# Optimization experiments

Measured on AMD Instinct MI355X. Metric: run time of the kernel, lower is better.

Reference implementation:

```python
import jax, jax.numpy as jnp
import numpy as np

NUM_EMBEDDINGS = 8192
EMBED_DIM = 64
NUM_BATCH = 4
N_VOX = 32768
EPS = 1e-10


def setup_inputs() -> dict:
    key = jax.random.key(0)
    k1, k2, k3, k4 = jax.random.split(key, 4)
    z_feats = jax.random.normal(k1, (N_VOX, EMBED_DIM), dtype=jnp.float32)
    batch_ids = jax.random.randint(k2, (N_VOX, 1), 0, NUM_BATCH)
    xyz = jax.random.randint(k3, (N_VOX, 3), 0, 64)
    z_coords = jnp.concatenate([batch_ids, xyz], axis=1).astype(jnp.int32)
    codebook = jax.random.normal(k4, (NUM_EMBEDDINGS, EMBED_DIM), dtype=jnp.float32)
    return {"z_feats": z_feats, "z_coords": z_coords, "codebook": codebook}


def reference(z_feats, z_coords, codebook):
    # squared euclidean distances [N, K]; argmin identical to torch.cdist argmin
    d2 = (jnp.sum(z_feats * z_feats, axis=1, keepdims=True)
          - 2.0 * (z_feats @ codebook.T)
          + jnp.sum(codebook * codebook, axis=1)[None, :])
    encoding_indices = jnp.argmin(d2, axis=1)              # [N]
    quantized = codebook[encoding_indices]                 # [N, D] gather

    # losses (gradient mode, use_ema_update=False)
    commitment_loss = jnp.mean((z_feats - jax.lax.stop_gradient(quantized)) ** 2)
    vq_loss = jnp.mean((quantized - jax.lax.stop_gradient(z_feats)) ** 2)

    # straight-through estimator
    quantized_st = z_feats + jax.lax.stop_gradient(quantized - z_feats)

    # per-sample codebook stats (vectorized over the batch dimension)
    batch_ids = z_coords[:, 0]
    counts = jnp.zeros((NUM_BATCH, NUM_EMBEDDINGS), jnp.float32).at[batch_ids, encoding_indices].add(1.0)
    per_sample_n = jnp.sum(counts, axis=1, keepdims=True)  # tokens per sample
    probs = counts / per_sample_n
    sample_entropy = -jnp.sum(probs * jnp.log(probs + EPS), axis=1)  # [B]
    avg_entropy = jnp.mean(sample_entropy)
    avg_perplexity = jnp.mean(jnp.exp(sample_entropy))
    avg_unique_count = jnp.mean(jnp.sum(counts > 0, axis=1).astype(jnp.float32))
    utilization_ratio = avg_unique_count / NUM_EMBEDDINGS * 100.0

    encoding_indices_st = encoding_indices.astype(jnp.float32)[:, None]
    return (quantized_st, vq_loss, commitment_loss, encoding_indices_st,
            avg_perplexity, avg_entropy, avg_unique_count, utilization_ratio)
```

## Files before the change

kernel.cpp:

```cpp
#include <hip/hip_runtime.h>
#include <math.h>

#define NUM_EMB 8192
#define DIM     64
#define NBATCH  4
#define NVOX    32768
#define TPB     256
#define NSPLIT  4
#define QENT    (NUM_EMB / NSPLIT)
#define CHUNK   128
#define CERT_EPS 0.015f
#define RCH     512

#define OFF_Q     0
#define OFF_VQ    2097152
#define OFF_COMM  2097153
#define OFF_IDX   2097154
#define OFF_PERP  2129922
#define OFF_ENT   2129923
#define OFF_UNIQ  2129924
#define OFF_UTIL  2129925

typedef __bf16 bf16x8 __attribute__((ext_vector_type(8)));
typedef float  f32x4  __attribute__((ext_vector_type(4)));

#define GLDS16(SRC, DST) __builtin_amdgcn_global_load_lds(                    \
        (const __attribute__((address_space(1))) void*)(SRC),                 \
        (__attribute__((address_space(3))) void*)(DST), 16, 0, 0)

__device__ __forceinline__ unsigned short f2bf(float f) {
    unsigned u = __float_as_uint(f);
    unsigned r = u + 0x7FFFu + ((u >> 16) & 1u);
    return (unsigned short)(r >> 16);
}
__device__ __forceinline__ float bf2f(unsigned short h) {
    return __uint_as_float(((unsigned)h) << 16);
}
__device__ __forceinline__ unsigned fmap(float f) {
    unsigned u = __float_as_uint(f);
    return (u & 0x80000000u) ? ~u : (u | 0x80000000u);
}

__global__ void prep_kernel(const float* __restrict__ cb,
                            unsigned short* __restrict__ cbh,
                            unsigned short* __restrict__ cbm,
                            float* __restrict__ cnp4,
                            unsigned* __restrict__ counts,
                            unsigned* __restrict__ misc,
                            unsigned long long* __restrict__ merge,
                            float* __restrict__ out) {
    int row = blockIdx.x * 4 + (threadIdx.x >> 6);
    int l   = threadIdx.x & 63;
    float f = cb[row * DIM + l];
    unsigned short hh = f2bf(f); float r1 = f - bf2f(hh);
    cbh[row * DIM + l] = hh;
    cbm[row * DIM + l] = f2bf(r1);
    float s = f * f;
#pragma unroll
    for (int o = 32; o > 0; o >>= 1) s += __shfl_xor(s, o, 64);
    if (l < 4) cnp4[row * 4 + l] = -0.5f * s;

    int gid = blockIdx.x * TPB + threadIdx.x;
    if (gid < NBATCH * NUM_EMB) counts[gid] = 0;
    if (gid >= 32768 && gid < 65536) merge[gid - 32768] = ~0ull;
    if (gid < 16) misc[gid] = 0;
    if (blockIdx.x == 0) {
        if (threadIdx.x < 2) out[OFF_VQ + threadIdx.x] = 0.f;
        if (threadIdx.x < 4) out[OFF_PERP + threadIdx.x] = 0.f;
    }
}

__global__ __launch_bounds__(TPB) void argmin_kernel(
        const float* __restrict__ z,
        const unsigned short* __restrict__ cbh,
        const unsigned short* __restrict__ cbm,
        const float* __restrict__ cnp4,
        float4* __restrict__ res) {
    __shared__ __align__(16) char lds[2 * CHUNK * 128 + CHUNK * 16];

    const int t  = threadIdx.x;
    const int l  = t & 63, w = t >> 6;
    const int lc = l & 15, lg = l >> 4;
    const int vb = blockIdx.x >> 2, qh = blockIdx.x & 3;
    const int ebase = qh * QENT;

    union U { bf16x8 v; unsigned short s[8]; };
    U Ah[2][2], Am[2][2];
#pragma unroll
    for (int set = 0; set < 2; ++set) {
        const float* zp = z + (size_t)(vb * 128 + w * 32 + set * 16 + lc) * DIM + lg * 8;
#pragma unroll
        for (int ks = 0; ks < 2; ++ks)
#pragma unroll
            for (int j = 0; j < 8; ++j) {
                float f = zp[ks * 32 + j];
                unsigned short hh = f2bf(f);
                Ah[set][ks].s[j] = hh;
                Am[set][ks].s[j] = f2bf(f - bf2f(hh));
            }
    }

    float m1[2][4], m2[2][4]; int ix[2][4];
#pragma unroll
    for (int set = 0; set < 2; ++set)
#pragma unroll
        for (int r = 0; r < 4; ++r) {
            m1[set][r] = -INFINITY; m2[set][r] = -INFINITY; ix[set][r] = 0;
        }

    const int b0 = (lc * 128 + lg * 16) ^ ((lc & 7) << 4);
    const int b1 = b0 ^ 64;
    const int cb0 = 2 * CHUNK * 128 + lc * 16;

    for (int ch = 0; ch < QENT / CHUNK; ++ch) {
        const char* sh = (const char*)cbh + (size_t)(ebase + ch * CHUNK) * 128;
        const char* sm = (const char*)cbm + (size_t)(ebase + ch * CHUNK) * 128;
#pragma unroll
        for (int j = 0; j < 4; ++j) {
            int lin = (j * 256 + t) * 16;
            int src = lin ^ (((lin >> 7) & 7) << 4);
            int dstb = lin - l * 16;
            GLDS16(sh + src, lds + dstb);
            GLDS16(sm + src, lds + 16384 + dstb);
        }
        if (t < 128) {
            int lin = t * 16;
            GLDS16((const char*)cnp4 + (size_t)(ebase + ch * CHUNK) * 16 + lin,
                   lds + 32768 + (lin - l * 16));
        }
        __syncthreads();

        int e0 = ebase + ch * CHUNK + lc;
        for (int tile = 0; tile < CHUNK / 16; ++tile) {
            bf16x8 bh0 = *(const bf16x8*)(lds + b0 + tile * 2048);
            bf16x8 bh1 = *(const bf16x8*)(lds + b1 + tile * 2048);
            bf16x8 bm0 = *(const bf16x8*)(lds + 16384 + b0 + tile * 2048);
            bf16x8 bm1 = *(const bf16x8*)(lds + 16384 + b1 + tile * 2048);
            f32x4  c0  = *(const f32x4*)(lds + cb0 + tile * 256);
            int eidx = e0 + tile * 16;
#pragma unroll
            for (int set = 0; set < 2; ++set) {
                f32x4 a = c0;
                a = __builtin_amdgcn_mfma_f32_16x16x32_bf16(Ah[set][0].v, bh0, a, 0, 0, 0);
                a = __builtin_amdgcn_mfma_f32_16x16x32_bf16(Am[set][0].v, bh0, a, 0, 0, 0);
                a = __builtin_amdgcn_mfma_f32_16x16x32_bf16(Ah[set][0].v, bm0, a, 0, 0, 0);
                a = __builtin_amdgcn_mfma_f32_16x16x32_bf16(Ah[set][1].v, bh1, a, 0, 0, 0);
                a = __builtin_amdgcn_mfma_f32_16x16x32_bf16(Am[set][1].v, bh1, a, 0, 0, 0);
                a = __builtin_amdgcn_mfma_f32_16x16x32_bf16(Ah[set][1].v, bm1, a, 0, 0, 0);
#pragma unroll
                for (int r = 0; r < 4; ++r) {
                    float v = a[r];
                    m2[set][r] = __builtin_amdgcn_fmed3f(v, m1[set][r], m2[set][r]);
                    if (v > m1[set][r]) { m1[set][r] = v; ix[set][r] = eidx; }
                }
            }
        }
        __syncthreads();
    }

#pragma unroll
    for (int set = 0; set < 2; ++set)
#pragma unroll
        for (int r = 0; r < 4; ++r) {
            float v1 = m1[set][r], v2 = m2[set][r]; int i1 = ix[set][r];
#pragma unroll
            for (int st = 1; st < 16; st <<= 1) {
                float o1 = __shfl_xor(v1, st, 16);
                float o2 = __shfl_xor(v2, st, 16);
                int   oi = __shfl_xor(i1, st, 16);
                float mn = fminf(v1, o1);
                v2 = fmaxf(fmaxf(v2, o2), mn);
                if (o1 > v1 || (o1 == v1 && oi < i1)) { v1 = o1; i1 = oi; }
            }
            if (lc == 0) {
                int vox = vb * 128 + w * 32 + set * 16 + lg * 4 + r;
                res[(size_t)qh * NVOX + vox] =
                    make_float4(v1, v2, __int_as_float(i1), 0.f);
            }
        }
}

__global__ void combine_kernel(const float4* __restrict__ res, float* __restrict__ out) {
    int vox = blockIdx.x * blockDim.x + threadIdx.x;
    float v1 = -INFINITY, v2 = -INFINITY; int idx = 0;
#pragma unroll
    for (int h = 0; h < NSPLIT; ++h) {
        float4 t4 = res[(size_t)h * NVOX + vox];
        float a1 = t4.x, a2 = t4.y; int ai = __float_as_int(t4.z);
        float mn = fminf(v1, a1);
        v2 = fmaxf(fmaxf(v2, a2), mn);
        if (a1 > v1) { v1 = a1; idx = ai; }
    }
    unsigned flag = (v1 - v2 < CERT_EPS) ? 0x80000000u : 0u;
    ((unsigned*)out)[OFF_IDX + vox] = (unsigned)idx | flag;
}

__global__ void gather_kernel(const float* __restrict__ z, const int* __restrict__ zc,
        const float* __restrict__ cb, float* __restrict__ out,
        unsigned* __restrict__ counts, float* __restrict__ sqsum,
        unsigned* __restrict__ list, unsigned* __restrict__ lcount) {
    int vox = blockIdx.x * blockDim.x + threadIdx.x;
    unsigned pk = ((unsigned*)out)[OFF_IDX + vox];
    float s = 0.f;
    if (pk & 0x80000000u) {
        unsigned pos = atomicAdd(lcount, 1u);
        list[pos] = vox;
    } else {
        unsigned idx = pk;
        const float4* crow = (const float4*)(cb + (size_t)idx * DIM);
        const float4* zrow = (const float4*)(z + (size_t)vox * DIM);
        float4* qrow = (float4*)(out + OFF_Q + (size_t)vox * DIM);
#pragma unroll
        for (int i = 0; i < DIM / 4; ++i) {
            float4 c4 = crow[i];
            float4 z4 = zrow[i];
            float dx = z4.x - c4.x, dy = z4.y - c4.y;
            float dz = z4.z - c4.z, dw = z4.w - c4.w;
            s += dx * dx + dy * dy + dz * dz + dw * dw;
            qrow[i] = c4;
        }
        out[OFF_IDX + vox] = (float)idx;
        atomicAdd(&counts[zc[vox * 4] * NUM_EMB + idx], 1u);
    }
#pragma unroll
    for (int o = 32; o > 0; o >>= 1) s += __shfl_down(s, o, 64);
    __shared__ float red[TPB / 64];
    if ((threadIdx.x & 63) == 0) red[threadIdx.x >> 6] = s;
    __syncthreads();
    if (threadIdx.x == 0)
        atomicAdd(sqsum, red[0] + red[1] + red[2] + red[3]);
}

__global__ void gatherF_kernel(const float* __restrict__ z, const int* __restrict__ zc,
        const float* __restrict__ cb, const float4* __restrict__ res,
        float* __restrict__ out, unsigned* __restrict__ counts,
        float* __restrict__ sqsum, unsigned* __restrict__ list,
        unsigned* __restrict__ lcount) {
    int vox = blockIdx.x * blockDim.x + threadIdx.x;
    float v1 = -INFINITY, v2 = -INFINITY; int idx = 0;
#pragma unroll
    for (int h = 0; h < NSPLIT; ++h) {
        float4 t4 = res[(size_t)h * NVOX + vox];
        float a1 = t4.x, a2 = t4.y; int ai = __float_as_int(t4.z);
        float mn = fminf(v1, a1);
        v2 = fmaxf(fmaxf(v2, a2), mn);
        if (a1 > v1) { v1 = a1; idx = ai; }
    }
    float s = 0.f;
    if (v1 - v2 < CERT_EPS) {
        unsigned pos = atomicAdd(lcount, 1u);
        list[pos] = vox;
    } else {
        const float4* crow = (const float4*)(cb + (size_t)idx * DIM);
        const float4* zrow = (const float4*)(z + (size_t)vox * DIM);
        float4* qrow = (float4*)(out + OFF_Q + (size_t)vox * DIM);
#pragma unroll
        for (int i = 0; i < DIM / 4; ++i) {
            float4 c4 = crow[i];
            float4 z4 = zrow[i];
            float dx = z4.x - c4.x, dy = z4.y - c4.y;
            float dz = z4.z - c4.z, dw = z4.w - c4.w;
            s += dx * dx + dy * dy + dz * dz + dw * dw;
            qrow[i] = c4;
        }
        out[OFF_IDX + vox] = (float)idx;
        atomicAdd(&counts[zc[vox * 4] * NUM_EMB + idx], 1u);
    }
#pragma unroll
    for (int o = 32; o > 0; o >>= 1) s += __shfl_down(s, o, 64);
    __shared__ float red[TPB / 64];
    if ((threadIdx.x & 63) == 0) red[threadIdx.x >> 6] = s;
    __syncthreads();
    if (threadIdx.x == 0)
        atomicAdd(sqsum, red[0] + red[1] + red[2] + red[3]);
}

__global__ void repair_scan_kernel(const float* __restrict__ z,
        const float* __restrict__ cb, const unsigned* __restrict__ list,
        const unsigned* __restrict__ lcount,
        unsigned long long* __restrict__ merge) {
    int wid = (blockIdx.x * blockDim.x + threadIdx.x) >> 6;
    int l   = threadIdx.x & 63;
    int nw  = (gridDim.x * blockDim.x) >> 6;
    int nitems = (int)*lcount * (NUM_EMB / RCH);
    int sub = l & 15, ent = l >> 4;

    for (int it = wid; it < nitems; it += nw) {
        int k    = it / (NUM_EMB / RCH);
        int base = (it % (NUM_EMB / RCH)) * RCH;
        int vox  = list[k];
        float4 z4 = ((const float4*)(z + (size_t)vox * DIM))[sub];
        float m = INFINITY; int mi = 0;

        for (int g0 = 0; g0 < RCH / 4; g0 += 4) {
            float d[4];
#pragma unroll
            for (int u = 0; u < 4; ++u) {
                int e = base + (g0 + u) * 4 + ent;
                float4 c4 = ((const float4*)(cb + (size_t)e * DIM))[sub];
                float dx = z4.x - c4.x, dy = z4.y - c4.y;
                float dz = z4.z - c4.z, dw = z4.w - c4.w;
                d[u] = fmaf(dx, dx, fmaf(dy, dy, fmaf(dz, dz, dw * dw)));
            }
#pragma unroll
            for (int st = 1; st < 16; st <<= 1)
#pragma unroll
                for (int u = 0; u < 4; ++u) d[u] += __shfl_xor(d[u], st, 16);
#pragma unroll
            for (int u = 0; u < 4; ++u) {
                int e = base + (g0 + u) * 4 + ent;
                if (d[u] < m) { m = d[u]; mi = e; }
            }
        }
#pragma unroll
        for (int st = 32; st > 0; st >>= 1) {
            float om = __shfl_xor(m, st, 64);
            int   oi = __shfl_xor(mi, st, 64);
            if (om < m || (om == m && oi < mi)) { m = om; mi = oi; }
        }
        if (l == 0) {
            unsigned long long key =
                ((unsigned long long)fmap(m) << 32) | (unsigned)mi;
            atomicMin(&merge[vox], key);
        }
    }
}

__global__ void repair_apply_kernel(const float* __restrict__ z,
        const int* __restrict__ zc, const float* __restrict__ cb,
        const unsigned* __restrict__ list, const unsigned* __restrict__ lcount,
        const unsigned long long* __restrict__ merge, float* __restrict__ out,
        unsigned* __restrict__ counts, float* __restrict__ sqsum) {
    int wid = (blockIdx.x * blockDim.x + threadIdx.x) >> 6;
    int l   = threadIdx.x & 63;
    int n   = (int)*lcount;
    int nw  = (gridDim.x * blockDim.x) >> 6;
    for (int k = wid; k < n; k += nw) {
        int vox = list[k];
        int mi  = (int)(merge[vox] & 0xFFFFFFFFull);
        float cv = cb[(size_t)mi * DIM + l];
        float zv = z[(size_t)vox * DIM + l];
        out[OFF_Q + (size_t)vox * DIM + l] = cv;
        float df = zv - cv;
        float s = df * df;
#pragma unroll
        for (int st = 32; st > 0; st >>= 1) s += __shfl_xor(s, st, 64);
        if (l == 0) {
            out[OFF_IDX + vox] = (float)mi;
            atomicAdd(&counts[zc[vox * 4] * NUM_EMB + mi], 1u);
            atomicAdd(sqsum, s);
        }
    }
}

__global__ void stats_final_kernel(const unsigned* __restrict__ counts,
                                   const float* __restrict__ sqsum,
                                   float* __restrict__ out) {
    int b = blockIdx.x;
    const unsigned* c = counts + b * NUM_EMB;

    __shared__ float sred[TPB / 64];
    float nf = 0.f;
    for (int i = threadIdx.x; i < NUM_EMB; i += TPB) nf += (float)c[i];
#pragma unroll
    for (int o = 32; o > 0; o >>= 1) nf += __shfl_down(nf, o, 64);
    if ((threadIdx.x & 63) == 0) sred[threadIdx.x >> 6] = nf;
    __syncthreads();
    float n = sred[0] + sred[1] + sred[2] + sred[3];
    __syncthreads();

    float ent = 0.f, uniq = 0.f;
    for (int i = threadIdx.x; i < NUM_EMB; i += TPB) {
        unsigned ci = c[i];
        if (ci) {
            float p = (float)ci / n;
            ent -= p * logf(p + 1e-10f);
            uniq += 1.f;
        }
    }
#pragma unroll
    for (int o = 32; o > 0; o >>= 1) {
        ent  += __shfl_down(ent, o, 64);
        uniq += __shfl_down(uniq, o, 64);
    }
    __shared__ float e4[TPB / 64], u4[TPB / 64];
    if ((threadIdx.x & 63) == 0) { e4[threadIdx.x >> 6] = ent; u4[threadIdx.x >> 6] = uniq; }
    __syncthreads();
    if (threadIdx.x == 0) {
        float eb = e4[0] + e4[1] + e4[2] + e4[3];
        float ub = u4[0] + u4[1] + u4[2] + u4[3];
        atomicAdd(&out[OFF_ENT],  eb * 0.25f);
        atomicAdd(&out[OFF_PERP], expf(eb) * 0.25f);
        atomicAdd(&out[OFF_UNIQ], ub * 0.25f);
        atomicAdd(&out[OFF_UTIL], ub * (100.f / (4.f * NUM_EMB)));
        if (b == 0) {
            float loss = *sqsum / (float)((size_t)NVOX * DIM);
            out[OFF_VQ]   = loss;
            out[OFF_COMM] = loss;
        }
    }
}

extern "C" void kernel_launch(void* const* d_in, const int* in_sizes, int n_in,
                              void* d_out, int out_size, void* d_ws, size_t ws_size,
                              hipStream_t stream) {
    const float* z  = (const float*)d_in[0];
    const int*   zc = (const int*)d_in[1];
    const float* cb = (const float*)d_in[2];
    float* out = (float*)d_out;
    char* ws = (char*)d_ws;

    unsigned short* cbh = (unsigned short*)out;
    unsigned short* cbm = cbh + NUM_EMB * DIM;

    unsigned* counts = (unsigned*)ws;
    unsigned* list   = (unsigned*)(ws + 131072);
    unsigned* misc   = (unsigned*)(ws + 262144);
    unsigned* lcount = misc;
    float*    sqsum  = (float*)(ws + 262148);
    float*    cnp4   = (float*)(ws + 262208);
    unsigned long long* merge = (unsigned long long*)(ws + 393280);
    size_t res_ws_off = 655424;
    bool bigws = ws_size >= res_ws_off + (size_t)NSPLIT * NVOX * 16;
    float4* res = bigws ? (float4*)(ws + res_ws_off)
                        : (float4*)(out + 524288);

    prep_kernel<<<NUM_EMB / 4, TPB, 0, stream>>>(cb, cbh, cbm, cnp4, counts,
                                                 misc, merge, out);
    argmin_kernel<<<(NVOX / 128) * NSPLIT, TPB, 0, stream>>>(z, cbh, cbm, cnp4, res);
    if (bigws) {
        gatherF_kernel<<<NVOX / TPB, TPB, 0, stream>>>(z, zc, cb, res, out,
                                                       counts, sqsum, list, lcount);
    } else {
        combine_kernel<<<NVOX / TPB, TPB, 0, stream>>>(res, out);
        gather_kernel<<<NVOX / TPB, TPB, 0, stream>>>(z, zc, cb, out, counts,
                                                      sqsum, list, lcount);
    }
    repair_scan_kernel<<<512, TPB, 0, stream>>>(z, cb, list, lcount, merge);
    repair_apply_kernel<<<64, TPB, 0, stream>>>(z, zc, cb, list, lcount, merge,
                                                out, counts, sqsum);
    stats_final_kernel<<<NBATCH, TPB, 0, stream>>>(counts, sqsum, out);
}
```

Measured before the change: 196.3 us.

## Double-buffer codebook chunks in LDS to overlap loads with MFMA compute

Measured after the change: 196.0 us. About the same (-0.2%).

```diff
diff --git a/kernel.cpp b/kernel.cpp
--- a/kernel.cpp
+++ b/kernel.cpp
@@ -8,7 +8,9 @@
 #define TPB     256
 #define NSPLIT  4
 #define QENT    (NUM_EMB / NSPLIT)
-#define CHUNK   128
+#define CHUNK   64
+#define NCH     (QENT / CHUNK)
+#define BUFSZ   (CHUNK * 128 * 2 + CHUNK * 16)
 #define CERT_EPS 0.015f
 #define RCH     512
 
@@ -76,7 +78,7 @@
         const unsigned short* __restrict__ cbm,
         const float* __restrict__ cnp4,
         float4* __restrict__ res) {
-    __shared__ __align__(16) char lds[2 * CHUNK * 128 + CHUNK * 16];
+    __shared__ __align__(16) char lds[2 * BUFSZ];
 
     const int t  = threadIdx.x;
     const int l  = t & 63, w = t >> 6;
@@ -110,33 +112,41 @@
 
     const int b0 = (lc * 128 + lg * 16) ^ ((lc & 7) << 4);
     const int b1 = b0 ^ 64;
-    const int cb0 = 2 * CHUNK * 128 + lc * 16;
-
-    for (int ch = 0; ch < QENT / CHUNK; ++ch) {
-        const char* sh = (const char*)cbh + (size_t)(ebase + ch * CHUNK) * 128;
-        const char* sm = (const char*)cbm + (size_t)(ebase + ch * CHUNK) * 128;
-#pragma unroll
-        for (int j = 0; j < 4; ++j) {
-            int lin = (j * 256 + t) * 16;
-            int src = lin ^ (((lin >> 7) & 7) << 4);
-            int dstb = lin - l * 16;
-            GLDS16(sh + src, lds + dstb);
-            GLDS16(sm + src, lds + 16384 + dstb);
-        }
-        if (t < 128) {
-            int lin = t * 16;
-            GLDS16((const char*)cnp4 + (size_t)(ebase + ch * CHUNK) * 16 + lin,
-                   lds + 32768 + (lin - l * 16));
-        }
-        __syncthreads();
+    const int cb0 = CHUNK * 256 + lc * 16;
+
+#define STAGE(CH, BUF) {                                                      \
+        const char* sh_ = (const char*)cbh + (size_t)(ebase + (CH) * CHUNK) * 128; \
+        const char* sm_ = (const char*)cbm + (size_t)(ebase + (CH) * CHUNK) * 128; \
+        _Pragma("unroll")                                                     \
+        for (int j = 0; j < 2; ++j) {                                         \
+            int lin = (j * 256 + t) * 16;                                     \
+            int src = lin ^ (((lin >> 7) & 7) << 4);                          \
+            int dstb = lin - l * 16;                                          \
+            GLDS16(sh_ + src, (BUF) + dstb);                                  \
+            GLDS16(sm_ + src, (BUF) + 8192 + dstb);                           \
+        }                                                                     \
+        if (t < CHUNK) {                                                      \
+            int lin = t * 16;                                                 \
+            GLDS16((const char*)cnp4 + (size_t)(ebase + (CH) * CHUNK) * 16 + lin, \
+                   (BUF) + 16384 + (lin - l * 16));                           \
+        }                                                                     \
+    }
+
+    STAGE(0, lds);
+    __syncthreads();
+
+    for (int ch = 0; ch < NCH; ++ch) {
+        char* cur = lds + (ch & 1) * BUFSZ;
+        if (ch + 1 < NCH) STAGE(ch + 1, lds + ((ch + 1) & 1) * BUFSZ);
 
         int e0 = ebase + ch * CHUNK + lc;
+#pragma unroll
         for (int tile = 0; tile < CHUNK / 16; ++tile) {
-            bf16x8 bh0 = *(const bf16x8*)(lds + b0 + tile * 2048);
-            bf16x8 bh1 = *(const bf16x8*)(lds + b1 + tile * 2048);
-            bf16x8 bm0 = *(const bf16x8*)(lds + 16384 + b0 + tile * 2048);
-            bf16x8 bm1 = *(const bf16x8*)(lds + 16384 + b1 + tile * 2048);
-            f32x4  c0  = *(const f32x4*)(lds + cb0 + tile * 256);
+            bf16x8 bh0 = *(const bf16x8*)(cur + b0 + tile * 2048);
+            bf16x8 bh1 = *(const bf16x8*)(cur + b1 + tile * 2048);
+            bf16x8 bm0 = *(const bf16x8*)(cur + 8192 + b0 + tile * 2048);
+            bf16x8 bm1 = *(const bf16x8*)(cur + 8192 + b1 + tile * 2048);
+            f32x4  c0  = *(const f32x4*)(cur + cb0 + tile * 256);
             int eidx = e0 + tile * 16;
 #pragma unroll
             for (int set = 0; set < 2; ++set) {
```
